# Performance work log

Hardware: AMD Instinct MI355X
Metric: run time of the kernel (lower is better)

Reference implementation:

```python
import jax, jax.numpy as jnp
import numpy as np

N = 8192   # num_neurons
P = 64     # num stored patterns


def setup_inputs() -> dict:
    key = jax.random.key(0)
    k1, k2 = jax.random.split(key)
    # Bipolar (+/-1) stored patterns, as in classical Hopfield usage
    X = jnp.where(jax.random.normal(k1, (N, P)) >= 0, 1.0, -1.0).astype(jnp.float32)
    # Initial (possibly corrupted) bipolar state
    state = jnp.where(jax.random.normal(k2, (N,)) >= 0, 1.0, -1.0).astype(jnp.float32)
    # Visit order for asynchronous updates (torch.randperm in original; any permutation is valid)
    perm = jnp.arange(N, dtype=jnp.int32)
    return {"X": X, "state": state, "perm": perm}


def reference(X, state, perm):
    n = X.shape[0]
    # W = X X^T / N with zero diagonal (Hebbian weights), as in __init__
    W = (X @ X.T) / n                                  # [N, N]
    W = W * (1.0 - jnp.eye(n, dtype=W.dtype))
    # Strictly sequential asynchronous update over the given permutation
    def step(s, i):
        act = jnp.dot(W[i], s)                         # dot(W[i], new_state)
        s = s.at[i].set(jnp.where(act >= 0, 1.0, -1.0).astype(s.dtype))
        return s, None
    final_state, _ = jax.lax.scan(step, state, perm)
    return final_state
```

## Files before the change

kernel.cpp:

```cpp
#include <hip/hip_runtime.h>
#include <stdint.h>


#define NB 128
typedef unsigned long long u64;


__global__ __launch_bounds__(256) void hop_prep(
    const float* __restrict__ X, const float* __restrict__ state,
    const int* __restrict__ perm, float* __restrict__ m0,
    float* __restrict__ Yt, u64* __restrict__ sig, u64* __restrict__ sigT,
    float* __restrict__ sps)
{
  const int b = blockIdx.x;
  const int t = threadIdx.x;
  const int wv = t >> 6, ln = t & 63;
  __shared__ u64 sigL[64];
  __shared__ float red[4][64];

  {
    const int j = t >> 2, qc = t & 3;
    const int r = perm[b*64 + j];
    const float s = state[r];
    const float4* xr = (const float4*)(X + (size_t)r*64) + qc*4;
    float4* yw = (float4*)Yt + (size_t)b*1024 + j;
    #pragma unroll
    for (int kk = 0; kk < 4; ++kk) {
      float4 x = xr[kk];
      float4 y; y.x = x.x*s; y.y = x.y*s; y.z = x.z*s; y.w = x.w*s;
      yw[(qc*4 + kk) * 64] = y;
    }
  }

  #pragma unroll
  for (int jj = 0; jj < 16; ++jj) {
    const int j = wv*16 + jj;
    const int r = perm[b*64 + j];
    u64 bb = __ballot(X[(size_t)r*64 + ln] < 0.f);
    if (state[r] < 0.f) bb = ~bb;
    if (ln == 0) { sig[b*64 + j] = bb; sigL[j] = bb; }
  }
  __syncthreads();

  {
    const u64 gs = sigL[ln];
    #pragma unroll
    for (int jj = 0; jj < 16; ++jj) {
      const int p = wv*16 + jj;
      u64 tb = __ballot((unsigned)((gs >> p) & 1ull));
      if (ln == 0) sigT[b*64 + p] = tb;
    }
  }

  {
    float acc = 0.f;
    for (int jj = 0; jj < 16; ++jj) {
      const int r = perm[b*64 + wv*16 + jj];
      acc = fmaf(X[(size_t)r*64 + ln], state[r], acc);
    }
    red[wv][ln] = acc;
    __syncthreads();
    if (t < 64) {
      atomicAdd(&m0[t], (red[0][t] + red[1][t]) + (red[2][t] + red[3][t]));
      sps[b*64 + t] = state[perm[b*64 + t]];
    }
  }
}

#define PROCESS(Y, gsig, gsigT, rr, ss) {                                     \
  float q0=0.f,q1=0.f,q2=0.f,q3=0.f;                                          \
  const float4* mv4 = (const float4*)mlds;                                    \
  _Pragma("unroll")                                                           \
  for (int g = 0; g < 16; ++g) {                                              \
    const float4 yv = Y[g]; const float4 mv = mv4[g];                         \
    q0 = fmaf(yv.x, mv.x, q0); q1 = fmaf(yv.y, mv.y, q1);                     \
    q2 = fmaf(yv.z, mv.z, q2); q3 = fmaf(yv.w, mv.w, q3);                     \
  }                                                                           \
  float q = ((q0+q1)+(q2+q3)) + ((ss < 0.f) ? -64.5f : -64.0f);               \
  u64 flips = 0ull, live = ~0ull;                                             \
  for (;;) {                                                                  \
    const u64 mm = __ballot(q < 0.f) & live;                                  \
    if (!mm) break;                                                           \
    const int i = (int)__builtin_ctzll(mm);                                   \
    flips |= (mm & (~mm + 1ull));                                             \
    live = (i < 63) ? ((~0ull) << (i + 1)) : 0ull;                            \
    const unsigned blo = (unsigned)__builtin_amdgcn_readlane((int)(unsigned)(gsig), i); \
    const unsigned bhi = (unsigned)__builtin_amdgcn_readlane((int)((gsig) >> 32), i);   \
    const u64 xb = (gsig) ^ (((u64)bhi << 32) | (u64)blo);                    \
    q = fmaf(4.0f, (float)__popcll(xb), q - 128.0f);                          \
  }                                                                           \
  if (flips) {                                                                \
    const int nf = (int)__popcll(flips);                                      \
    const int pc = (int)__popcll(flips & (gsigT));                            \
    mreg += (float)(4*pc - 2*nf);                                             \
    mlds[lane] = mreg;                                                        \
  }                                                                           \
  out[rr] = ((flips >> lane) & 1ull) ? -(ss) : (ss);                          \
}

__global__ __launch_bounds__(64) void hop_solve(
    const int* __restrict__ perm, const float* __restrict__ m0,
    const float4* __restrict__ Yt4, const u64* __restrict__ sig,
    const u64* __restrict__ sigT, const float* __restrict__ sps,
    float* __restrict__ out)
{
  __shared__ __align__(16) float mlds[64];
  const int lane = threadIdx.x;

  float mreg = m0[lane];
  mlds[lane] = mreg;

  float4 Ya[16], Yb[16];
  u64 sgA, stA, sgB, stB; int rA, rB; float sA, sB;

  {
    const float4* yp = Yt4 + lane;
    #pragma unroll
    for (int g = 0; g < 16; ++g) Ya[g] = yp[g*64];
    sgA = sig[lane]; stA = sigT[lane]; rA = perm[lane]; sA = sps[lane];
  }

  for (int bb = 0; bb < NB; bb += 2) {
    {
      const int bn = bb + 1;
      const float4* yp = Yt4 + (size_t)bn*1024 + lane;
      #pragma unroll
      for (int g = 0; g < 16; ++g) Yb[g] = yp[g*64];
      sgB = sig[bn*64+lane]; stB = sigT[bn*64+lane];
      rB = perm[bn*64+lane]; sB = sps[bn*64+lane];
    }
    PROCESS(Ya, sgA, stA, rA, sA);
    {
      const int bn = (bb + 2 < NB) ? bb + 2 : NB - 1;
      const float4* yp = Yt4 + (size_t)bn*1024 + lane;
      #pragma unroll
      for (int g = 0; g < 16; ++g) Ya[g] = yp[g*64];
      sgA = sig[bn*64+lane]; stA = sigT[bn*64+lane];
      rA = perm[bn*64+lane]; sA = sps[bn*64+lane];
    }
    PROCESS(Yb, sgB, stB, rB, sB);
  }
}

extern "C" void kernel_launch(void* const* d_in, const int* in_sizes, int n_in,
                              void* d_out, int out_size, void* d_ws, size_t ws_size,
                              hipStream_t stream) {
  const float* X     = (const float*)d_in[0];
  const float* state = (const float*)d_in[1];
  const int*   perm  = (const int*)d_in[2];
  float* outp = (float*)d_out;

  float* m0  = (float*)d_ws;
  float* Yt  = m0 + 64;
  u64*   sig = (u64*)(Yt + 128*4096);
  u64*   sigT= sig + 8192;
  float* sps = (float*)(sigT + 8192);

  hipMemsetAsync(m0, 0, 64*sizeof(float), stream);
  hop_prep<<<dim3(NB), dim3(256), 0, stream>>>(X, state, perm, m0, Yt, sig, sigT, sps);
  hop_solve<<<dim3(1), dim3(64), 0, stream>>>(perm, m0, (const float4*)Yt, sig, sigT, sps, outp);
}
```

Measured before the change: 453.2 us.

## Hand-code the sequential flip loop in inline asm with integer thresholds; fuse prep passes

The per-block sequential flip resolution loop in hop_solve is rewritten as hand-written GCN assembly. It uses integer activations and an incrementing threshold in an SGPR, which replaces the float ballot, ctz and mask logic and shortens the serial dependency chain of each flip iteration. The prep kernel now reads X and state once per element to produce the Yt layout, the signatures and the m0 partial sums together, instead of making three separate passes. Inline asm depends on wave64 behaviour and correct constraint handling. Truncating the activation to int assumes it is integral, which holds for bipolar inputs.

```diff
diff --git a/kernel.cpp b/kernel.cpp
--- a/kernel.cpp
+++ b/kernel.cpp
@@ -4,6 +4,7 @@
 
 #define NB 128
 typedef unsigned long long u64;
+typedef unsigned u32;
 
 
 __global__ __launch_bounds__(256) void hop_prep(
@@ -12,34 +13,25 @@
     float* __restrict__ Yt, u64* __restrict__ sig, u64* __restrict__ sigT,
     float* __restrict__ sps)
 {
-  const int b = blockIdx.x;
-  const int t = threadIdx.x;
+  const int b = blockIdx.x, t = threadIdx.x;
   const int wv = t >> 6, ln = t & 63;
   __shared__ u64 sigL[64];
   __shared__ float red[4][64];
 
-  {
-    const int j = t >> 2, qc = t & 3;
-    const int r = perm[b*64 + j];
-    const float s = state[r];
-    const float4* xr = (const float4*)(X + (size_t)r*64) + qc*4;
-    float4* yw = (float4*)Yt + (size_t)b*1024 + j;
-    #pragma unroll
-    for (int kk = 0; kk < 4; ++kk) {
-      float4 x = xr[kk];
-      float4 y; y.x = x.x*s; y.y = x.y*s; y.z = x.z*s; y.w = x.w*s;
-      yw[(qc*4 + kk) * 64] = y;
-    }
-  }
-
+  float acc = 0.f;
   #pragma unroll
   for (int jj = 0; jj < 16; ++jj) {
     const int j = wv*16 + jj;
     const int r = perm[b*64 + j];
-    u64 bb = __ballot(X[(size_t)r*64 + ln] < 0.f);
-    if (state[r] < 0.f) bb = ~bb;
+    const float sr = state[r];
+    const float x = X[(size_t)r*64 + ln];
+    Yt[(size_t)b*4096 + (ln >> 2)*256 + j*4 + (ln & 3)] = x * sr;
+    u64 bb = __ballot(x < 0.f);
+    if (sr < 0.f) bb = ~bb;
     if (ln == 0) { sig[b*64 + j] = bb; sigL[j] = bb; }
+    acc = fmaf(x, sr, acc);
   }
+  red[wv][ln] = acc;
   __syncthreads();
 
   {
@@ -52,18 +44,9 @@
     }
   }
 
-  {
-    float acc = 0.f;
-    for (int jj = 0; jj < 16; ++jj) {
-      const int r = perm[b*64 + wv*16 + jj];
-      acc = fmaf(X[(size_t)r*64 + ln], state[r], acc);
-    }
-    red[wv][ln] = acc;
-    __syncthreads();
-    if (t < 64) {
-      atomicAdd(&m0[t], (red[0][t] + red[1][t]) + (red[2][t] + red[3][t]));
-      sps[b*64 + t] = state[perm[b*64 + t]];
-    }
+  if (t < 64) {
+    atomicAdd(&m0[t], (red[0][t] + red[1][t]) + (red[2][t] + red[3][t]));
+    sps[b*64 + t] = state[perm[b*64 + t]];
   }
 }
 
@@ -76,18 +59,39 @@
     q0 = fmaf(yv.x, mv.x, q0); q1 = fmaf(yv.y, mv.y, q1);                     \
     q2 = fmaf(yv.z, mv.z, q2); q3 = fmaf(yv.w, mv.w, q3);                     \
   }                                                                           \
-  float q = ((q0+q1)+(q2+q3)) + ((ss < 0.f) ? -64.5f : -64.0f);               \
-  u64 flips = 0ull, live = ~0ull;                                             \
-  for (;;) {                                                                  \
-    const u64 mm = __ballot(q < 0.f) & live;                                  \
-    if (!mm) break;                                                           \
-    const int i = (int)__builtin_ctzll(mm);                                   \
-    flips |= (mm & (~mm + 1ull));                                             \
-    live = (i < 63) ? ((~0ull) << (i + 1)) : 0ull;                            \
-    const unsigned blo = (unsigned)__builtin_amdgcn_readlane((int)(unsigned)(gsig), i); \
-    const unsigned bhi = (unsigned)__builtin_amdgcn_readlane((int)((gsig) >> 32), i);   \
-    const u64 xb = (gsig) ^ (((u64)bhi << 32) | (u64)blo);                    \
-    q = fmaf(4.0f, (float)__popcll(xb), q - 128.0f);                          \
+  const float qf = (q0+q1)+(q2+q3);                 \
+  int T = ((int)qf << 1) - (((ss) < 0.f) ? 1 : 0);                            \
+  u64 flips;                                                                  \
+  {                                                                           \
+    const u32 siglo = (u32)(gsig), sighi = (u32)((gsig) >> 32);               \
+    int thr = 128;                                                            \
+    u64 live, mm, bit; u32 i_, t0, t1, v0, v1;                                \
+    asm volatile(                                                             \
+      "s_mov_b64 %[flips], 0\n\t"                                             \
+      "s_mov_b64 %[live], -1\n\t"                                             \
+      "1:\n\t"                                                                \
+      "v_cmp_gt_i32 vcc, %[thr], %[T]\n\t"                     \
+      "s_and_b64 %[mm], vcc, %[live]\n\t"                       \
+      "s_cbranch_scc0 2f\n\t"                                                 \
+      "s_ff1_i32_b64 %[i], %[mm]\n\t"                                         \
+      "v_readlane_b32 %[t0], %[siglo], %[i]\n\t"                              \
+      "v_readlane_b32 %[t1], %[sighi], %[i]\n\t"                              \
+      "s_lshl_b64 %[bit], 1, %[i]\n\t"               \
+      "s_or_b64 %[flips], %[flips], %[bit]\n\t"      \
+      "s_lshl_b64 %[live], -2, %[i]\n\t"             \
+      "s_addk_i32 %[thr], 0x100\n\t"                          \
+      "v_xor_b32 %[v0], %[t0], %[siglo]\n\t"                                  \
+      "v_xor_b32 %[v1], %[t1], %[sighi]\n\t"                                  \
+      "v_bcnt_u32_b32 %[v0], %[v0], 0\n\t"                                    \
+      "v_bcnt_u32_b32 %[v0], %[v1], %[v0]\n\t"                                \
+      "v_lshl_add_u32 %[T], %[v0], 3, %[T]\n\t"              \
+      "s_branch 1b\n\t"                                                       \
+      "2:\n\t"                                                                \
+      : [flips]"=&s"(flips), [live]"=&s"(live), [mm]"=&s"(mm),                \
+        [bit]"=&s"(bit), [i]"=&s"(i_), [t0]"=&s"(t0), [t1]"=&s"(t1),          \
+        [thr]"+s"(thr), [T]"+v"(T), [v0]"=&v"(v0), [v1]"=&v"(v1)              \
+      : [siglo]"v"(siglo), [sighi]"v"(sighi)                                  \
+      : "vcc", "scc");                                                        \
   }                                                                           \
   if (flips) {                                                                \
     const int nf = (int)__popcll(flips);                                      \
```

Result: faster. 368.2 us (-18.8%).
